# Kernel tuning notes

Measured on AMD Instinct MI355X. Metric: run time of the kernel, lower is better.

The kernel has to match this reference:

```python
import jax, jax.numpy as jnp
import numpy as np
import math

D = 2048
NH = 16
HD = D // NH
MULT = 4
EPS = 1e-6


def rmsnorm(x, g):
    norm = jax.lax.rsqrt(jnp.mean(x * x, axis=-1, keepdims=True) + EPS)
    return g * x * norm


def setup_inputs() -> dict:
    key = jax.random.key(0)
    ks = jax.random.split(key, 8)
    s = 0.02  # keep activations in a sane range
    return {
        "x": jax.random.normal(ks[0], (2, 2048, D), dtype=jnp.float32),
        "g1": jnp.ones((D,), dtype=jnp.float32),
        "wq": jax.random.normal(ks[1], (D, D), dtype=jnp.float32) * s,
        "wk": jax.random.normal(ks[2], (D, D), dtype=jnp.float32) * s,
        "wv": jax.random.normal(ks[3], (D, D), dtype=jnp.float32) * s,
        "wo": jax.random.normal(ks[4], (D, D), dtype=jnp.float32) * s,
        "g2": jnp.ones((D,), dtype=jnp.float32),
        "w_up": jax.random.normal(ks[5], (2 * D * MULT, D), dtype=jnp.float32) * s,
        "w_down": jax.random.normal(ks[6], (D, D * MULT), dtype=jnp.float32) * s,
    }


def reference(x, g1, wq, wk, wv, wo, g2, w_up, w_down):
    B, T, _ = x.shape
    # --- causal self-attention with pre-RMSNorm ---
    h = rmsnorm(x, g1)
    q = (h @ wq.T).reshape(B, T, NH, HD).transpose(0, 2, 1, 3)  # [B,H,T,hd]
    k = (h @ wk.T).reshape(B, T, NH, HD).transpose(0, 2, 1, 3)
    v = (h @ wv.T).reshape(B, T, NH, HD).transpose(0, 2, 1, 3)
    att = jnp.einsum("bhtd,bhsd->bhts", q, k) / math.sqrt(HD)  # [B,H,T,T]
    neg = jnp.finfo(att.dtype).min
    causal = jnp.triu(jnp.full((T, T), neg, dtype=att.dtype), k=1)
    att = att + causal
    w = jax.nn.softmax(att, axis=-1)
    z = jnp.einsum("bhts,bhsd->bhtd", w, v)  # [B,H,T,hd]
    z = z.transpose(0, 2, 1, 3).reshape(B, T, D)
    x = x + z @ wo.T
    # --- SwiGLU-style FFN (GELU gate) with pre-RMSNorm ---
    h2 = rmsnorm(x, g2)
    uv = h2 @ w_up.T  # [B,T,2*D*MULT]
    u, vgate = jnp.split(uv, 2, axis=-1)
    ff = (jax.nn.gelu(u, approximate=False) * vgate) @ w_down.T
    return x + ff
```

## Files before the change

kernel.cpp:

```cpp
#include <hip/hip_runtime.h>
#include <math.h>

typedef __bf16 bf16_t;
typedef __bf16 bf16x8 __attribute__((ext_vector_type(8)));
typedef __bf16 bf16x4 __attribute__((ext_vector_type(4)));
typedef float f32x4 __attribute__((ext_vector_type(4)));

#define D_MODEL 2048
#define N_HEADS 16
#define HEAD_D 128
#define SEQ 2048
#define NTOK 4096
#define DFF 8192
#define UPN 16384

#define GLDS16(g, l) __builtin_amdgcn_global_load_lds( \
    (const __attribute__((address_space(1))) void*)(g), \
    (__attribute__((address_space(3))) void*)(l), 16, 0, 0)

__global__ __launch_bounds__(256) void cvt_bf16_kernel(const float* __restrict__ in,
                                                       bf16_t* __restrict__ out, long n4) {
    long i = (long)blockIdx.x * 256 + threadIdx.x;
    long stride = (long)gridDim.x * 256;
    for (; i < n4; i += stride) {
        float4 f = ((const float4*)in)[i];
        bf16x4 v;
        v[0] = (bf16_t)f.x; v[1] = (bf16_t)f.y; v[2] = (bf16_t)f.z; v[3] = (bf16_t)f.w;
        ((bf16x4*)out)[i] = v;
    }
}

__global__ __launch_bounds__(256) void rmsnorm_kernel(const float* __restrict__ x,
                                                      const float* __restrict__ g,
                                                      bf16_t* __restrict__ out) {
    int row = blockIdx.x;
    const float* xr = x + (size_t)row * D_MODEL;
    int c0 = threadIdx.x * 8;
    float4 a = *(const float4*)&xr[c0];
    float4 b = *(const float4*)&xr[c0 + 4];
    float ss = a.x*a.x + a.y*a.y + a.z*a.z + a.w*a.w
             + b.x*b.x + b.y*b.y + b.z*b.z + b.w*b.w;
    #pragma unroll
    for (int off = 1; off < 64; off <<= 1) ss += __shfl_xor(ss, off);
    __shared__ float red[4];
    if ((threadIdx.x & 63) == 0) red[threadIdx.x >> 6] = ss;
    __syncthreads();
    float norm = rsqrtf((red[0] + red[1] + red[2] + red[3]) * (1.f / D_MODEL) + 1e-6f);
    float4 ga = *(const float4*)&g[c0];
    float4 gb = *(const float4*)&g[c0 + 4];
    bf16x8 o;
    o[0] = (bf16_t)(a.x * ga.x * norm); o[1] = (bf16_t)(a.y * ga.y * norm);
    o[2] = (bf16_t)(a.z * ga.z * norm); o[3] = (bf16_t)(a.w * ga.w * norm);
    o[4] = (bf16_t)(b.x * gb.x * norm); o[5] = (bf16_t)(b.y * gb.y * norm);
    o[6] = (bf16_t)(b.z * gb.z * norm); o[7] = (bf16_t)(b.w * gb.w * norm);
    *(bf16x8*)&out[(size_t)row * D_MODEL + c0] = o;
}

__device__ __forceinline__ void stage_half(const bf16_t* gbase, int ldK,
                                           bf16_t* lds_half, int wave, int lane) {
    #pragma unroll
    for (int i = 0; i < 2; ++i) {
        int rl = i * 64 + wave * 8 + (lane >> 3);
        int cb = ((lane & 7) ^ (lane >> 3)) << 4;
        const char* src = (const char*)(gbase + (size_t)rl * ldK) + cb;
        char* dst = (char*)lds_half + i * 8192 + wave * 1024;
        GLDS16(src, dst);
    }
}

template<int MODE>
__global__ __launch_bounds__(512)
void gemm8(const bf16_t* __restrict__ A, const bf16_t* __restrict__ W,
           void* __restrict__ o0, void* __restrict__ o1, void* __restrict__ o2,
           const float* __restrict__ res, int nbx, int K)
{
    __shared__ __align__(16) bf16_t As[2][256 * 64];
    __shared__ __align__(16) bf16_t Bs[2][(MODE == 2 ? 2 : 1) * 128 * 64];

    const int tid = threadIdx.x;
    const int wave = tid >> 6, lane = tid & 63;
    const int lr = lane & 15, lg = lane >> 4;
    const int wm = wave >> 1, wn = wave & 1;

    const int nwg = gridDim.x, bid = blockIdx.x;
    const int cpx = nwg >> 3;
    const int s = (bid & 7) * cpx + (bid >> 3);
    const int bx = s % nbx, by = s / nbx;
    const int bm0 = by * 256, bn0 = bx * 128;

    const bf16_t* Asrc0 = A + (size_t)bm0 * K;
    const bf16_t* Asrc1 = A + (size_t)(bm0 + 128) * K;
    const bf16_t* Bsrc0 = W + (size_t)bn0 * K;
    const bf16_t* Bsrc1 = (MODE == 2) ? (W + (size_t)(DFF + bn0) * K) : nullptr;

    auto issue = [&](int t) {
        int p = t & 1;
        size_t k0 = (size_t)t * 64;
        stage_half(Asrc0 + k0, K, &As[p][0], wave, lane);
        stage_half(Asrc1 + k0, K, &As[p][128 * 64], wave, lane);
        stage_half(Bsrc0 + k0, K, &Bs[p][0], wave, lane);
        if constexpr (MODE == 2)
            stage_half(Bsrc1 + k0, K, &Bs[p][128 * 64], wave, lane);
    };

    f32x4 accu[4][4] = {};
    f32x4 accv[4][4] = {};

    const int NKT = K >> 6;
    issue(0);
    for (int j = 0; j < NKT; ++j) {
        if (j + 1 < NKT) {
            issue(j + 1);
            if constexpr (MODE == 2) asm volatile("s_waitcnt vmcnt(8)" ::: "memory");
            else                     asm volatile("s_waitcnt vmcnt(6)" ::: "memory");
        } else {
            asm volatile("s_waitcnt vmcnt(0)" ::: "memory");
        }
        __builtin_amdgcn_s_barrier();

        const bf16_t* Ap = &As[j & 1][0];
        const bf16_t* Bp = &Bs[j & 1][0];

        bf16x8 af[4][2];
        #pragma unroll
        for (int m = 0; m < 4; ++m) {
            int row = wm * 64 + m * 16 + lr;
            #pragma unroll
            for (int kk = 0; kk < 2; ++kk)
                af[m][kk] = *(const bf16x8*)&Ap[row * 64 + ((kk * 32 + lg * 8) ^ ((row & 7) << 3))];
        }

        #pragma unroll
        for (int qn = 0; qn < 2; ++qn) {
            if constexpr (MODE != 2) {
                bf16x8 bfr[2][2];
                #pragma unroll
                for (int n2 = 0; n2 < 2; ++n2) {
                    int brow = wn * 64 + (qn * 2 + n2) * 16 + lr;
                    #pragma unroll
                    for (int kk = 0; kk < 2; ++kk)
                        bfr[n2][kk] = *(const bf16x8*)&Bp[brow * 64 + ((kk * 32 + lg * 8) ^ ((brow & 7) << 3))];
                }
                __builtin_amdgcn_s_setprio(1);
                #pragma unroll
                for (int m = 0; m < 4; ++m)
                    #pragma unroll
                    for (int n2 = 0; n2 < 2; ++n2)
                        #pragma unroll
                        for (int kk = 0; kk < 2; ++kk)
                            accu[m][qn * 2 + n2] = __builtin_amdgcn_mfma_f32_16x16x32_bf16(
                                af[m][kk], bfr[n2][kk], accu[m][qn * 2 + n2], 0, 0, 0);
                __builtin_amdgcn_s_setprio(0);
                __builtin_amdgcn_s_barrier();
            } else {
                #pragma unroll
                for (int qv = 0; qv < 2; ++qv) {
                    const bf16_t* Bpq = Bp + qv * (128 * 64);
                    bf16x8 bfr[2][2];
                    #pragma unroll
                    for (int n2 = 0; n2 < 2; ++n2) {
                        int brow = wn * 64 + (qn * 2 + n2) * 16 + lr;
                        #pragma unroll
                        for (int kk = 0; kk < 2; ++kk)
                            bfr[n2][kk] = *(const bf16x8*)&Bpq[brow * 64 + ((kk * 32 + lg * 8) ^ ((brow & 7) << 3))];
                    }
                    f32x4 (*accp)[4] = qv ? accv : accu;
                    __builtin_amdgcn_s_setprio(1);
                    #pragma unroll
                    for (int m = 0; m < 4; ++m)
                        #pragma unroll
                        for (int n2 = 0; n2 < 2; ++n2)
                            #pragma unroll
                            for (int kk = 0; kk < 2; ++kk)
                                accp[m][qn * 2 + n2] = __builtin_amdgcn_mfma_f32_16x16x32_bf16(
                                    af[m][kk], bfr[n2][kk], accp[m][qn * 2 + n2], 0, 0, 0);
                    __builtin_amdgcn_s_setprio(0);
                    __builtin_amdgcn_s_barrier();
                }
            }
        }
    }

    const int r0 = lg * 4;
    if constexpr (MODE == 0) {
        const float qs = 0.08838834764831845f;
        const int th = bn0 >> 11;
        #pragma unroll
        for (int m = 0; m < 4; ++m) {
            int grow = bm0 + wm * 64 + m * 16 + r0;
            #pragma unroll
            for (int n = 0; n < 4; ++n) {
                int gcol = bn0 + wn * 64 + n * 16 + lr;
                int c = gcol & 2047;
                if (th == 0) {
                    #pragma unroll
                    for (int r = 0; r < 4; ++r)
                        ((bf16_t*)o0)[(size_t)(grow + r) * D_MODEL + c] = (bf16_t)(accu[m][n][r] * qs);
                } else if (th == 1) {
                    #pragma unroll
                    for (int r = 0; r < 4; ++r)
                        ((bf16_t*)o1)[(size_t)(grow + r) * D_MODEL + c] = (bf16_t)accu[m][n][r];
                } else {
                    int hh = c >> 7, d = c & 127;
                    int bb = grow >> 11, t0 = grow & 2047;
                    bf16x4 st;
                    #pragma unroll
                    for (int r = 0; r < 4; ++r) st[r] = (bf16_t)accu[m][n][r];
                    *(bf16x4*)&((bf16_t*)o2)[((size_t)(bb * N_HEADS + hh) * HEAD_D + d) * SEQ + t0] = st;
                }
            }
        }
    } else if constexpr (MODE == 1) {
        #pragma unroll
        for (int m = 0; m < 4; ++m) {
            int grow = bm0 + wm * 64 + m * 16 + r0;
            #pragma unroll
            for (int n = 0; n < 4; ++n) {
                int gcol = bn0 + wn * 64 + n * 16 + lr;
                #pragma unroll
                for (int r = 0; r < 4; ++r) {
                    size_t idx = (size_t)(grow + r) * D_MODEL + gcol;
                    ((float*)o0)[idx] = res[idx] + accu[m][n][r];
                }
            }
        }
    } else {
        #pragma unroll
        for (int m = 0; m < 4; ++m) {
            int grow = bm0 + wm * 64 + m * 16 + r0;
            #pragma unroll
            for (int n = 0; n < 4; ++n) {
                int gcol = bn0 + wn * 64 + n * 16 + lr;
                #pragma unroll
                for (int r = 0; r < 4; ++r) {
                    float u = accu[m][n][r], vg = accv[m][n][r];
                    float ge = 0.5f * u * (1.f + erff(u * 0.70710678118654752f));
                    ((bf16_t*)o0)[(size_t)(grow + r) * DFF + gcol] = (bf16_t)(ge * vg);
                }
            }
        }
    }
}

__global__ __launch_bounds__(256)
void attn_kernel(const bf16_t* __restrict__ Q, const bf16_t* __restrict__ K,
                 const bf16_t* __restrict__ Vt, bf16_t* __restrict__ Z)
{
    const int qt = gridDim.x - 1 - blockIdx.x;
    const int h = blockIdx.y, b = blockIdx.z;
    const int q0 = qt * 64;
    const int tid = threadIdx.x, wave = tid >> 6, lane = tid & 63;
    const int lr = lane & 15, lg = lane >> 4;

    __shared__ __align__(16) bf16_t Qs[64 * 136];
    __shared__ __align__(16) bf16_t Ks[64 * 136];
    __shared__ __align__(16) bf16_t Vts[128 * 72];
    __shared__ __align__(16) bf16_t Ps[4][16 * 72];

    const size_t base = ((size_t)b * SEQ) * D_MODEL + (size_t)h * HEAD_D;
    const size_t vbase = (size_t)(b * N_HEADS + h) * HEAD_D * SEQ;

    #pragma unroll
    for (int i = 0; i < 4; ++i) {
        int v = tid + 256 * i;
        int row = v >> 4, cv = (v & 15) * 8;
        *(uint4*)&Qs[row * 136 + cv] = *(const uint4*)&Q[base + (size_t)(q0 + row) * D_MODEL + cv];
    }

    f32x4 o[8] = {};
    float mrun[4], lrun[4];
    #pragma unroll
    for (int r = 0; r < 4; ++r) { mrun[r] = -1e30f; lrun[r] = 0.f; }

    for (int kt = 0; kt <= qt; ++kt) {
        const int k0 = kt * 64;
        __syncthreads();
        #pragma unroll
        for (int i = 0; i < 4; ++i) {
            int v = tid + 256 * i;
            int row = v >> 4, cv = (v & 15) * 8;
            *(uint4*)&Ks[row * 136 + cv] = *(const uint4*)&K[base + (size_t)(k0 + row) * D_MODEL + cv];
            int d = v >> 3, c8 = (v & 7) * 8;
            *(uint4*)&Vts[d * 72 + c8] = *(const uint4*)&Vt[vbase + (size_t)d * SEQ + k0 + c8];
        }
        __syncthreads();

        f32x4 s[4] = {};
        #pragma unroll
        for (int kk = 0; kk < 4; ++kk) {
            bf16x8 aq = *(const bf16x8*)&Qs[(wave * 16 + lr) * 136 + kk * 32 + lg * 8];
            #pragma unroll
            for (int nb = 0; nb < 4; ++nb) {
                bf16x8 bk = *(const bf16x8*)&Ks[(nb * 16 + lr) * 136 + kk * 32 + lg * 8];
                s[nb] = __builtin_amdgcn_mfma_f32_16x16x32_bf16(aq, bk, s[nb], 0, 0, 0);
            }
        }
        if (kt == qt) {
            #pragma unroll
            for (int nb = 0; nb < 4; ++nb)
                #pragma unroll
                for (int r = 0; r < 4; ++r) {
                    int qrel = 16 * wave + lg * 4 + r;
                    int krel = nb * 16 + lr;
                    if (krel > qrel) s[nb][r] = -1e30f;
                }
        }
        float resc[4];
        #pragma unroll
        for (int r = 0; r < 4; ++r) {
            float mx = fmaxf(fmaxf(s[0][r], s[1][r]), fmaxf(s[2][r], s[3][r]));
            #pragma unroll
            for (int off = 1; off < 16; off <<= 1) mx = fmaxf(mx, __shfl_xor(mx, off));
            float mnew = fmaxf(mrun[r], mx);
            resc[r] = __expf(mrun[r] - mnew);
            float sum = 0.f;
            #pragma unroll
            for (int nb = 0; nb < 4; ++nb) {
                float p = __expf(s[nb][r] - mnew);
                s[nb][r] = p;
                sum += p;
            }
            #pragma unroll
            for (int off = 1; off < 16; off <<= 1) sum += __shfl_xor(sum, off);
            lrun[r] = lrun[r] * resc[r] + sum;
            mrun[r] = mnew;
        }
        #pragma unroll
        for (int ob = 0; ob < 8; ++ob)
            #pragma unroll
            for (int r = 0; r < 4; ++r) o[ob][r] *= resc[r];
        #pragma unroll
        for (int nb = 0; nb < 4; ++nb)
            #pragma unroll
            for (int r = 0; r < 4; ++r)
                Ps[wave][(lg * 4 + r) * 72 + nb * 16 + lr] = (bf16_t)s[nb][r];
        #pragma unroll
        for (int kk = 0; kk < 2; ++kk) {
            bf16x8 ap = *(const bf16x8*)&Ps[wave][lr * 72 + kk * 32 + lg * 8];
            #pragma unroll
            for (int ob = 0; ob < 8; ++ob) {
                bf16x8 bv = *(const bf16x8*)&Vts[(ob * 16 + lr) * 72 + kk * 32 + lg * 8];
                o[ob] = __builtin_amdgcn_mfma_f32_16x16x32_bf16(ap, bv, o[ob], 0, 0, 0);
            }
        }
    }
    #pragma unroll
    for (int ob = 0; ob < 8; ++ob)
        #pragma unroll
        for (int r = 0; r < 4; ++r) {
            int t = q0 + 16 * wave + lg * 4 + r;
            Z[base + (size_t)t * D_MODEL + ob * 16 + lr] = (bf16_t)(o[ob][r] / lrun[r]);
        }
}

extern "C" void kernel_launch(void* const* d_in, const int* in_sizes, int n_in,
                              void* d_out, int out_size, void* d_ws, size_t ws_size,
                              hipStream_t stream)
{
    const float* x   = (const float*)d_in[0];
    const float* g1  = (const float*)d_in[1];
    const float* wq  = (const float*)d_in[2];
    const float* wk  = (const float*)d_in[3];
    const float* wv  = (const float*)d_in[4];
    const float* wo  = (const float*)d_in[5];
    const float* g2  = (const float*)d_in[6];
    const float* wup = (const float*)d_in[7];
    const float* wdn = (const float*)d_in[8];
    float* out = (float*)d_out;

    char* wsp = (char*)d_ws;
    size_t off = 0;
    auto alloc = [&](size_t bytes) { void* p = wsp + off; off += (bytes + 255) & ~255ull; return p; };
    bf16_t* wq_b  = (bf16_t*)alloc((size_t)D_MODEL * D_MODEL * 2);
    bf16_t* wk_b  = (bf16_t*)alloc((size_t)D_MODEL * D_MODEL * 2);
    bf16_t* wv_b  = (bf16_t*)alloc((size_t)D_MODEL * D_MODEL * 2);
    bf16_t* wo_b  = (bf16_t*)alloc((size_t)D_MODEL * D_MODEL * 2);
    bf16_t* wup_b = (bf16_t*)alloc((size_t)UPN * D_MODEL * 2);
    bf16_t* wdn_b = (bf16_t*)alloc((size_t)D_MODEL * DFF * 2);
    bf16_t* h_b   = (bf16_t*)alloc((size_t)NTOK * D_MODEL * 2);
    bf16_t* q_b   = (bf16_t*)alloc((size_t)NTOK * D_MODEL * 2);
    bf16_t* k_b   = (bf16_t*)alloc((size_t)NTOK * D_MODEL * 2);
    bf16_t* vt_b  = (bf16_t*)alloc((size_t)NTOK * D_MODEL * 2);
    bf16_t* z_b   = (bf16_t*)alloc((size_t)NTOK * D_MODEL * 2);
    float*  x1    = (float*) alloc((size_t)NTOK * D_MODEL * 4);
    bf16_t* h2_b  = (bf16_t*)alloc((size_t)NTOK * D_MODEL * 2);
    bf16_t* act_b = (bf16_t*)alloc((size_t)NTOK * DFF * 2);

    auto cvt = [&](const float* in, bf16_t* outb, long n) {
        long n4 = n / 4;
        long nb = (n4 + 255) / 256;
        int blocks = nb > 2048 ? 2048 : (int)nb;
        cvt_bf16_kernel<<<blocks, 256, 0, stream>>>(in, outb, n4);
    };
    cvt(wq,  wq_b,  (long)D_MODEL * D_MODEL);
    cvt(wk,  wk_b,  (long)D_MODEL * D_MODEL);
    cvt(wv,  wv_b,  (long)D_MODEL * D_MODEL);
    cvt(wo,  wo_b,  (long)D_MODEL * D_MODEL);
    cvt(wup, wup_b, (long)UPN * D_MODEL);
    cvt(wdn, wdn_b, (long)D_MODEL * DFF);

    rmsnorm_kernel<<<NTOK, 256, 0, stream>>>(x, g1, h_b);

    gemm8<0><<<48 * 16, 512, 0, stream>>>(h_b, wq_b, q_b, k_b, vt_b, nullptr, 48, D_MODEL);

    attn_kernel<<<dim3(SEQ / 64, N_HEADS, 2), 256, 0, stream>>>(q_b, k_b, vt_b, z_b);

    gemm8<1><<<16 * 16, 512, 0, stream>>>(z_b, wo_b, x1, nullptr, nullptr, x, 16, D_MODEL);

    rmsnorm_kernel<<<NTOK, 256, 0, stream>>>(x1, g2, h2_b);

    gemm8<2><<<64 * 16, 512, 0, stream>>>(h2_b, wup_b, act_b, nullptr, nullptr, nullptr, 64, D_MODEL);

    gemm8<1><<<16 * 16, 512, 0, stream>>>(act_b, wdn_b, out, nullptr, nullptr, x1, 16, DFF);
}
```

Measured before the change: 1.023 ms.

## Switch GEMMs to 256x256 tiles with half-K staging and split-K down projection

Replaces the 256x128 GEMM with a 256x256 tile kernel (8 waves arranged 2x4, 64-wide K steps loaded as two 32-wide halves, new XOR swizzle). The gate/up GEMM now loads interleaved u/v weight rows into one B tile. The goal is more data reuse per LDS load and fewer blocks re-reading operands. The down projection becomes split-K (2 partials), with a separate combine kernel that adds the residual, and the partial buffer reuses dead workspace starting at h_b. The cost is an extra pass over memory for the combine, and the Wo GEMM now launches only 128 blocks, which may leave CUs idle.

```diff
diff --git a/kernel.cpp b/kernel.cpp
--- a/kernel.cpp
+++ b/kernel.cpp
@@ -17,6 +17,8 @@
 #define GLDS16(g, l) __builtin_amdgcn_global_load_lds( \
     (const __attribute__((address_space(1))) void*)(g), \
     (__attribute__((address_space(3))) void*)(l), 16, 0, 0)
+
+#define MFMA16(a, b, c) __builtin_amdgcn_mfma_f32_16x16x32_bf16((a), (b), (c), 0, 0, 0)
 
 __global__ __launch_bounds__(256) void cvt_bf16_kernel(const float* __restrict__ in,
                                                        bf16_t* __restrict__ out, long n4) {
@@ -56,138 +58,125 @@
     *(bf16x8*)&out[(size_t)row * D_MODEL + c0] = o;
 }
 
-__device__ __forceinline__ void stage_half(const bf16_t* gbase, int ldK,
-                                           bf16_t* lds_half, int wave, int lane) {
-    #pragma unroll
-    for (int i = 0; i < 2; ++i) {
-        int rl = i * 64 + wave * 8 + (lane >> 3);
-        int cb = ((lane & 7) ^ (lane >> 3)) << 4;
-        const char* src = (const char*)(gbase + (size_t)rl * ldK) + cb;
-        char* dst = (char*)lds_half + i * 8192 + wave * 1024;
-        GLDS16(src, dst);
-    }
-}
-
-template<int MODE>
-__global__ __launch_bounds__(512)
-void gemm8(const bf16_t* __restrict__ A, const bf16_t* __restrict__ W,
-           void* __restrict__ o0, void* __restrict__ o1, void* __restrict__ o2,
-           const float* __restrict__ res, int nbx, int K)
+__global__ __launch_bounds__(256) void combine3_kernel(const float* __restrict__ r,
+        const float* __restrict__ p0, const float* __restrict__ p1,
+        float* __restrict__ out, long n4) {
+    long i = (long)blockIdx.x * 256 + threadIdx.x;
+    long stride = (long)gridDim.x * 256;
+    for (; i < n4; i += stride) {
+        float4 a = ((const float4*)r)[i];
+        float4 b = ((const float4*)p0)[i];
+        float4 c = ((const float4*)p1)[i];
+        float4 o; o.x = a.x+b.x+c.x; o.y = a.y+b.y+c.y; o.z = a.z+b.z+c.z; o.w = a.w+b.w+c.w;
+        ((float4*)out)[i] = o;
+    }
+}
+
+template<int MODE, int KSPLIT>
+__global__ __launch_bounds__(512, 2)
+void gemm256(const bf16_t* __restrict__ A, const bf16_t* __restrict__ W,
+             void* __restrict__ o0, void* __restrict__ o1, void* __restrict__ o2,
+             const float* __restrict__ res, int nbx, int K)
 {
-    __shared__ __align__(16) bf16_t As[2][256 * 64];
-    __shared__ __align__(16) bf16_t Bs[2][(MODE == 2 ? 2 : 1) * 128 * 64];
-
+    __shared__ __align__(16) bf16_t ldsA[4 * 8192];
+    __shared__ __align__(16) bf16_t ldsB[4 * 8192];
     const int tid = threadIdx.x;
     const int wave = tid >> 6, lane = tid & 63;
     const int lr = lane & 15, lg = lane >> 4;
-    const int wm = wave >> 1, wn = wave & 1;
+    const int wm = wave >> 2, wn = wave & 3;
 
     const int nwg = gridDim.x, bid = blockIdx.x;
     const int cpx = nwg >> 3;
     const int s = (bid & 7) * cpx + (bid >> 3);
-    const int bx = s % nbx, by = s / nbx;
-    const int bm0 = by * 256, bn0 = bx * 128;
-
-    const bf16_t* Asrc0 = A + (size_t)bm0 * K;
-    const bf16_t* Asrc1 = A + (size_t)(bm0 + 128) * K;
-    const bf16_t* Bsrc0 = W + (size_t)bn0 * K;
-    const bf16_t* Bsrc1 = (MODE == 2) ? (W + (size_t)(DFF + bn0) * K) : nullptr;
-
-    auto issue = [&](int t) {
-        int p = t & 1;
-        size_t k0 = (size_t)t * 64;
-        stage_half(Asrc0 + k0, K, &As[p][0], wave, lane);
-        stage_half(Asrc1 + k0, K, &As[p][128 * 64], wave, lane);
-        stage_half(Bsrc0 + k0, K, &Bs[p][0], wave, lane);
-        if constexpr (MODE == 2)
-            stage_half(Bsrc1 + k0, K, &Bs[p][128 * 64], wave, lane);
+    const int by = s & 15, bx = s >> 4;
+    const int bm0 = by * 256;
+    const int bn0 = (MODE == 2) ? bx * 128 : bx * 256;
+    const int z = (KSPLIT == 2) ? blockIdx.z : 0;
+    const int Keff = K / KSPLIT;
+    const int koff = z * Keff;
+
+    const int rl0 = wave * 16 + (lane >> 2);
+    const int Lof = ((lane & 3) ^ ((rl0 >> 1) & 3)) * 8;
+    const bf16_t* asrc0 = A + (size_t)(bm0 + rl0) * K + koff + Lof;
+    const bf16_t* asrc1 = asrc0 + (size_t)128 * K;
+    const bf16_t* bsrc0;
+    const bf16_t* bsrc1;
+    if constexpr (MODE == 2) {
+        int grp = rl0 >> 6, wi = rl0 & 63;
+        int brow = (wi < 32) ? (bn0 + grp * 32 + wi) : (DFF + bn0 + grp * 32 + (wi - 32));
+        bsrc0 = W + (size_t)brow * K + koff + Lof;
+        bsrc1 = bsrc0 + (size_t)64 * K;
+    } else {
+        bsrc0 = W + (size_t)(bn0 + rl0) * K + koff + Lof;
+        bsrc1 = bsrc0 + (size_t)128 * K;
+    }
+
+    auto issueA = [&](int t, int kh) {
+        char* dst = (char*)ldsA + (((t & 1) * 2 + kh) * 16384) + wave * 1024;
+        const bf16_t* sp = asrc0 + (size_t)t * 64 + kh * 32;
+        GLDS16(sp, dst);
+        GLDS16(asrc1 + (size_t)t * 64 + kh * 32, dst + 8192);
     };
-
-    f32x4 accu[4][4] = {};
-    f32x4 accv[4][4] = {};
-
-    const int NKT = K >> 6;
-    issue(0);
-    for (int j = 0; j < NKT; ++j) {
-        if (j + 1 < NKT) {
-            issue(j + 1);
-            if constexpr (MODE == 2) asm volatile("s_waitcnt vmcnt(8)" ::: "memory");
-            else                     asm volatile("s_waitcnt vmcnt(6)" ::: "memory");
-        } else {
-            asm volatile("s_waitcnt vmcnt(0)" ::: "memory");
-        }
-        __builtin_amdgcn_s_barrier();
-
-        const bf16_t* Ap = &As[j & 1][0];
-        const bf16_t* Bp = &Bs[j & 1][0];
-
-        bf16x8 af[4][2];
-        #pragma unroll
-        for (int m = 0; m < 4; ++m) {
-            int row = wm * 64 + m * 16 + lr;
-            #pragma unroll
-            for (int kk = 0; kk < 2; ++kk)
-                af[m][kk] = *(const bf16x8*)&Ap[row * 64 + ((kk * 32 + lg * 8) ^ ((row & 7) << 3))];
-        }
-
-        #pragma unroll
-        for (int qn = 0; qn < 2; ++qn) {
-            if constexpr (MODE != 2) {
-                bf16x8 bfr[2][2];
-                #pragma unroll
-                for (int n2 = 0; n2 < 2; ++n2) {
-                    int brow = wn * 64 + (qn * 2 + n2) * 16 + lr;
-                    #pragma unroll
-                    for (int kk = 0; kk < 2; ++kk)
-                        bfr[n2][kk] = *(const bf16x8*)&Bp[brow * 64 + ((kk * 32 + lg * 8) ^ ((brow & 7) << 3))];
-                }
-                __builtin_amdgcn_s_setprio(1);
-                #pragma unroll
-                for (int m = 0; m < 4; ++m)
-                    #pragma unroll
-                    for (int n2 = 0; n2 < 2; ++n2)
-                        #pragma unroll
-                        for (int kk = 0; kk < 2; ++kk)
-                            accu[m][qn * 2 + n2] = __builtin_amdgcn_mfma_f32_16x16x32_bf16(
-                                af[m][kk], bfr[n2][kk], accu[m][qn * 2 + n2], 0, 0, 0);
-                __builtin_amdgcn_s_setprio(0);
-                __builtin_amdgcn_s_barrier();
-            } else {
-                #pragma unroll
-                for (int qv = 0; qv < 2; ++qv) {
-                    const bf16_t* Bpq = Bp + qv * (128 * 64);
-                    bf16x8 bfr[2][2];
-                    #pragma unroll
-                    for (int n2 = 0; n2 < 2; ++n2) {
-                        int brow = wn * 64 + (qn * 2 + n2) * 16 + lr;
-                        #pragma unroll
-                        for (int kk = 0; kk < 2; ++kk)
-                            bfr[n2][kk] = *(const bf16x8*)&Bpq[brow * 64 + ((kk * 32 + lg * 8) ^ ((brow & 7) << 3))];
-                    }
-                    f32x4 (*accp)[4] = qv ? accv : accu;
-                    __builtin_amdgcn_s_setprio(1);
-                    #pragma unroll
-                    for (int m = 0; m < 4; ++m)
-                        #pragma unroll
-                        for (int n2 = 0; n2 < 2; ++n2)
-                            #pragma unroll
-                            for (int kk = 0; kk < 2; ++kk)
-                                accp[m][qn * 2 + n2] = __builtin_amdgcn_mfma_f32_16x16x32_bf16(
-                                    af[m][kk], bfr[n2][kk], accp[m][qn * 2 + n2], 0, 0, 0);
-                    __builtin_amdgcn_s_setprio(0);
-                    __builtin_amdgcn_s_barrier();
-                }
-            }
-        }
-    }
-
-    const int r0 = lg * 4;
+    auto issueB = [&](int t, int kh) {
+        char* dst = (char*)ldsB + (((t & 1) * 2 + kh) * 16384) + wave * 1024;
+        GLDS16(bsrc0 + (size_t)t * 64 + kh * 32, dst);
+        GLDS16(bsrc1 + (size_t)t * 64 + kh * 32, dst + 8192);
+    };
+
+    f32x4 acc[8][4] = {};
+    const int xg = (lg ^ ((lr >> 1) & 3)) * 8;
+    const int arow = wm * 128 + lr;
+    const int brow = wn * 64 + lr;
+    const int NKT = Keff >> 6;
+
+    issueA(0, 0); issueB(0, 0); issueA(0, 1); issueB(0, 1);
+
+#define HALF_BODY(J, ISSUE, KH, WC)                                                     \
+    {                                                                                   \
+        bf16x8 af[8], bfr[2];                                                           \
+        const bf16_t* Ar = ldsA + (((J) & 1) * 2 + (KH)) * 8192;                        \
+        const bf16_t* Br = ldsB + (((J) & 1) * 2 + (KH)) * 8192;                        \
+        if (ISSUE) issueA((J) + 1, (KH));                                               \
+        asm volatile("s_waitcnt vmcnt(" WC ")" ::: "memory");                           \
+        __builtin_amdgcn_s_barrier();                                                   \
+        _Pragma("unroll")                                                               \
+        for (int m = 0; m < 8; ++m) af[m] = *(const bf16x8*)&Ar[(arow + m * 16) * 32 + xg]; \
+        _Pragma("unroll")                                                               \
+        for (int n = 0; n < 2; ++n) bfr[n] = *(const bf16x8*)&Br[(brow + n * 16) * 32 + xg]; \
+        __builtin_amdgcn_s_setprio(1);                                                  \
+        _Pragma("unroll")                                                               \
+        for (int m = 0; m < 8; ++m) {                                                   \
+            acc[m][0] = MFMA16(af[m], bfr[0], acc[m][0]);                               \
+            acc[m][1] = MFMA16(af[m], bfr[1], acc[m][1]);                               \
+        }                                                                               \
+        __builtin_amdgcn_s_setprio(0);                                                  \
+        if (ISSUE) issueB((J) + 1, (KH));                                               \
+        _Pragma("unroll")                                                               \
+        for (int n = 0; n < 2; ++n) bfr[n] = *(const bf16x8*)&Br[(brow + (n + 2) * 16) * 32 + xg]; \
+        __builtin_amdgcn_s_setprio(1);                                                  \
+        _Pragma("unroll")                                                               \
+        for (int m = 0; m < 8; ++m) {                                                   \
+            acc[m][2] = MFMA16(af[m], bfr[0], acc[m][2]);                               \
+            acc[m][3] = MFMA16(af[m], bfr[1], acc[m][3]);                               \
+        }                                                                               \
+        __builtin_amdgcn_s_setprio(0);                                                  \
+        __builtin_amdgcn_s_barrier();                                                   \
+    }
+
+    for (int j = 0; j < NKT - 1; ++j) {
+        HALF_BODY(j, true, 0, "6");
+        HALF_BODY(j, true, 1, "6");
+    }
+    HALF_BODY(NKT - 1, false, 0, "4");
+    HALF_BODY(NKT - 1, false, 1, "0");
+#undef HALF_BODY
+
     if constexpr (MODE == 0) {
         const float qs = 0.08838834764831845f;
         const int th = bn0 >> 11;
         #pragma unroll
-        for (int m = 0; m < 4; ++m) {
-            int grow = bm0 + wm * 64 + m * 16 + r0;
+        for (int m = 0; m < 8; ++m) {
+            int grow = bm0 + wm * 128 + m * 16 + lg * 4;
             #pragma unroll
             for (int n = 0; n < 4; ++n) {
                 int gcol = bn0 + wn * 64 + n * 16 + lr;
@@ -195,45 +184,47 @@
                 if (th == 0) {
                     #pragma unroll
                     for (int r = 0; r < 4; ++r)
-                        ((bf16_t*)o0)[(size_t)(grow + r) * D_MODEL + c] = (bf16_t)(accu[m][n][r] * qs);
+                        ((bf16_t*)o0)[(size_t)(grow + r) * D_MODEL + c] = (bf16_t)(acc[m][n][r] * qs);
                 } else if (th == 1) {
                     #pragma unroll
                     for (int r = 0; r < 4; ++r)
-                        ((bf16_t*)o1)[(size_t)(grow + r) * D_MODEL + c] = (bf16_t)accu[m][n][r];
+                        ((bf16_t*)o1)[(size_t)(grow + r) * D_MODEL + c] = (bf16_t)acc[m][n][r];
                 } else {
                     int hh = c >> 7, d = c & 127;
                     int bb = grow >> 11, t0 = grow & 2047;
                     bf16x4 st;
                     #pragma unroll
-                    for (int r = 0; r < 4; ++r) st[r] = (bf16_t)accu[m][n][r];
+                    for (int r = 0; r < 4; ++r) st[r] = (bf16_t)acc[m][n][r];
                     *(bf16x4*)&((bf16_t*)o2)[((size_t)(bb * N_HEADS + hh) * HEAD_D + d) * SEQ + t0] = st;
                 }
             }
         }
     } else if constexpr (MODE == 1) {
-        #pragma unroll
-        for (int m = 0; m < 4; ++m) {
-            int grow = bm0 + wm * 64 + m * 16 + r0;
+        float* po = (KSPLIT == 2) ? ((float*)o0 + (size_t)z * NTOK * D_MODEL) : (float*)o0;
+        #pragma unroll
+        for (int m = 0; m < 8; ++m) {
+            int grow = bm0 + wm * 128 + m * 16 + lg * 4;
             #pragma unroll
             for (int n = 0; n < 4; ++n) {
                 int gcol = bn0 + wn * 64 + n * 16 + lr;
                 #pragma unroll
                 for (int r = 0; r < 4; ++r) {
                     size_t idx = (size_t)(grow + r) * D_MODEL + gcol;
-                    ((float*)o0)[idx] = res[idx] + accu[m][n][r];
+                    if (KSPLIT == 2) po[idx] = acc[m][n][r];
+                    else             po[idx] = res[idx] + acc[m][n][r];
                 }
             }
         }
     } else {
         #pragma unroll
-        for (int m = 0; m < 4; ++m) {
-            int grow = bm0 + wm * 64 + m * 16 + r0;
-            #pragma unroll
-            for (int n = 0; n < 4; ++n) {
-                int gcol = bn0 + wn * 64 + n * 16 + lr;
+        for (int m = 0; m < 8; ++m) {
+            int grow = bm0 + wm * 128 + m * 16 + lg * 4;
+            #pragma unroll
+            for (int n = 0; n < 2; ++n) {
+                int gcol = bn0 + wn * 32 + n * 16 + lr;
                 #pragma unroll
                 for (int r = 0; r < 4; ++r) {
-                    float u = accu[m][n][r], vg = accv[m][n][r];
+                    float u = acc[m][n][r], vg = acc[m][n + 2][r];
                     float ge = 0.5f * u * (1.f + erff(u * 0.70710678118654752f));
                     ((bf16_t*)o0)[(size_t)(grow + r) * DFF + gcol] = (bf16_t)(ge * vg);
                 }
@@ -285,14 +276,14 @@
         }
         __syncthreads();
 
-        f32x4 s[4] = {};
+        f32x4 sv[4] = {};
         #pragma unroll
         for (int kk = 0; kk < 4; ++kk) {
             bf16x8 aq = *(const bf16x8*)&Qs[(wave * 16 + lr) * 136 + kk * 32 + lg * 8];
             #pragma unroll
             for (int nb = 0; nb < 4; ++nb) {
                 bf16x8 bk = *(const bf16x8*)&Ks[(nb * 16 + lr) * 136 + kk * 32 + lg * 8];
-                s[nb] = __builtin_amdgcn_mfma_f32_16x16x32_bf16(aq, bk, s[nb], 0, 0, 0);
+                sv[nb] = MFMA16(aq, bk, sv[nb]);
             }
         }
         if (kt == qt) {
@@ -302,13 +293,13 @@
                 for (int r = 0; r < 4; ++r) {
                     int qrel = 16 * wave + lg * 4 + r;
                     int krel = nb * 16 + lr;
-                    if (krel > qrel) s[nb][r] = -1e30f;
+                    if (krel > qrel) sv[nb][r] = -1e30f;
                 }
         }
         float resc[4];
         #pragma unroll
         for (int r = 0; r < 4; ++r) {
-            float mx = fmaxf(fmaxf(s[0][r], s[1][r]), fmaxf(s[2][r], s[3][r]));
+            float mx = fmaxf(fmaxf(sv[0][r], sv[1][r]), fmaxf(sv[2][r], sv[3][r]));
             #pragma unroll
             for (int off = 1; off < 16; off <<= 1) mx = fmaxf(mx, __shfl_xor(mx, off));
             float mnew = fmaxf(mrun[r], mx);
@@ -316,8 +307,8 @@
             float sum = 0.f;
             #pragma unroll
             for (int nb = 0; nb < 4; ++nb) {
-                float p = __expf(s[nb][r] - mnew);
-                s[nb][r] = p;
+                float p = __expf(sv[nb][r] - mnew);
+                sv[nb][r] = p;
                 sum += p;
             }
             #pragma unroll
@@ -333,14 +324,14 @@
         for (int nb = 0; nb < 4; ++nb)
             #pragma unroll
             for (int r = 0; r < 4; ++r)
-                Ps[wave][(lg * 4 + r) * 72 + nb * 16 + lr] = (bf16_t)s[nb][r];
+                Ps[wave][(lg * 4 + r) * 72 + nb * 16 + lr] = (bf16_t)sv[nb][r];
         #pragma unroll
         for (int kk = 0; kk < 2; ++kk) {
             bf16x8 ap = *(const bf16x8*)&Ps[wave][lr * 72 + kk * 32 + lg * 8];
             #pragma unroll
             for (int ob = 0; ob < 8; ++ob) {
                 bf16x8 bv = *(const bf16x8*)&Vts[(ob * 16 + lr) * 72 + kk * 32 + lg * 8];
-                o[ob] = __builtin_amdgcn_mfma_f32_16x16x32_bf16(ap, bv, o[ob], 0, 0, 0);
+                o[ob] = MFMA16(ap, bv, o[ob]);
             }
         }
     }
@@ -385,6 +376,7 @@
     float*  x1    = (float*) alloc((size_t)NTOK * D_MODEL * 4);
     bf16_t* h2_b  = (bf16_t*)alloc((size_t)NTOK * D_MODEL * 2);
     bf16_t* act_b = (bf16_t*)alloc((size_t)NTOK * DFF * 2);
+    float* pbuf = (float*)h_b;
 
     auto cvt = [&](const float* in, bf16_t* outb, long n) {
         long n4 = n / 4;
@@ -401,15 +393,17 @@
 
     rmsnorm_kernel<<<NTOK, 256, 0, stream>>>(x, g1, h_b);
 
-    gemm8<0><<<48 * 16, 512, 0, stream>>>(h_b, wq_b, q_b, k_b, vt_b, nullptr, 48, D_MODEL);
+    gemm256<0, 1><<<24 * 16, 512, 0, stream>>>(h_b, wq_b, q_b, k_b, vt_b, nullptr, 24, D_MODEL);
 
     attn_kernel<<<dim3(SEQ / 64, N_HEADS, 2), 256, 0, stream>>>(q_b, k_b, vt_b, z_b);
 
-    gemm8<1><<<16 * 16, 512, 0, stream>>>(z_b, wo_b, x1, nullptr, nullptr, x, 16, D_MODEL);
+    gemm256<1, 1><<<8 * 16, 512, 0, stream>>>(z_b, wo_b, x1, nullptr, nullptr, x, 8, D_MODEL);
 
     rmsnorm_kernel<<<NTOK, 256, 0, stream>>>(x1, g2, h2_b);
 
-    gemm8<2><<<64 * 16, 512, 0, stream>>>(h2_b, wup_b, act_b, nullptr, nullptr, nullptr, 64, D_MODEL);
-
-    gemm8<1><<<16 * 16, 512, 0, stream>>>(act_b, wdn_b, out, nullptr, nullptr, x1, 16, DFF);
-}
+    gemm256<2, 1><<<64 * 16, 512, 0, stream>>>(h2_b, wup_b, act_b, nullptr, nullptr, nullptr, 64, D_MODEL);
+
+    gemm256<1, 2><<<dim3(8 * 16, 1, 2), 512, 0, stream>>>(act_b, wdn_b, pbuf, nullptr, nullptr, nullptr, 8, DFF);
+    combine3_kernel<<<2048, 256, 0, stream>>>(x1, pbuf, pbuf + (size_t)NTOK * D_MODEL, out,
+                                              (long)NTOK * D_MODEL / 4);
+}
```

Result: slower. 1.076 ms (+5.2%).
